# Optimization experiments

Measured on AMD Instinct MI355X. Metric: run time of the kernel, lower is better.

The kernel has to match this reference:

```python
import jax, jax.numpy as jnp
import numpy as np

B, T, U = 1024, 256, 256  # batch, timesteps, units (= input_dim)


def setup_inputs() -> dict:
    key = jax.random.key(0)
    ks = jax.random.split(key, 8)
    g = lambda k, shape: (jax.random.normal(k, shape, dtype=jnp.float32)
                          * np.float32(np.sqrt(2.0 / sum(shape if len(shape) > 1 else (shape[0], 1)))))
    return {
        "inputs": jax.random.normal(ks[0], (B, T, U), dtype=jnp.float32),
        "embedding_kernel": g(ks[1], (U, U)),
        "state_kernel": g(ks[2], (U, U)),
        "bias": g(ks[3], (U,)),
        "length_kernel": g(ks[4], (U, 1)),
        "rnn_state_kernel": g(ks[5], (U, 3 * U)),
        "rnn_embedding_kernel": g(ks[6], (U, 3 * U)),
        "rnn_newin_kernel": g(ks[7], (U, 3 * U)),
    }


def reference(inputs, embedding_kernel, state_kernel, bias, length_kernel,
              rnn_state_kernel, rnn_embedding_kernel, rnn_newin_kernel):
    u = state_kernel.shape[0]
    b = inputs.shape[0]

    def step(carry, x):
        state, s1, s2 = carry                       # each (B, U)
        query = state @ state_kernel                # (B, U)
        value = jnp.stack([s1, s2, x], axis=1)      # (B, 3, U) -- 3 memory slots
        emb = jnp.einsum('bsu,uv->bsv', value, embedding_kernel)
        act = jnp.tanh(emb + query[:, None, :] + bias)          # (B, 3, U)
        scores = jnp.einsum('bsu,u->bs', act, length_kernel[:, 0])  # (B, 3)
        prob = jax.nn.softmax(scores, axis=1)
        attention_out = jnp.einsum('bsu,bs->bu', value, prob)   # (B, U)

        gs = state @ rnn_state_kernel               # (B, 3U)
        ge = attention_out @ rnn_embedding_kernel   # (B, 3U)
        gn = x @ rnn_newin_kernel                   # (B, 3U)
        u_p = jax.nn.sigmoid(gs[:, :u] + ge[:, :u] + gn[:, :u])
        r_p = jax.nn.sigmoid(gs[:, u:2*u] + ge[:, u:2*u] + gn[:, u:2*u])
        cand = jnp.tanh(r_p * gs[:, 2*u:] + ge[:, 2*u:] + gn[:, 2*u:])
        step_out = (1.0 - u_p) * state + u_p * cand
        # state update mirrors Keras: [step_out, states[2], step_in]
        return (step_out, s2, x), None

    init = (jnp.zeros((b, u), inputs.dtype),
            jnp.zeros((b, u), inputs.dtype),
            jnp.zeros((b, u), inputs.dtype))
    xs = jnp.swapaxes(inputs, 0, 1)  # (T, B, U)
    (last_out, _, _), _ = jax.lax.scan(step, init, xs)
    return last_out  # (B, U) -- K.rnn's last_output
```

## Files before the change

kernel.cpp:

```cpp
#include <hip/hip_runtime.h>


typedef _Float16 f16;
typedef _Float16 f16x8 __attribute__((ext_vector_type(8)));
typedef _Float16 f16x4 __attribute__((ext_vector_type(4)));
typedef float f32x4 __attribute__((ext_vector_type(4)));

static __device__ __forceinline__ f32x4 mfma16(f16x8 a, f16x8 b, f32x4 c){
  return __builtin_amdgcn_mfma_f32_16x16x32_f16(a, b, c, 0, 0, 0);
}
static __device__ __forceinline__ float sigmoid_f(float x){
  return 1.0f / (1.0f + __expf(-x));
}
static __device__ __forceinline__ float tanh_f(float x){
  float e = __expf(2.0f * x);
  return 1.0f - 2.0f / (e + 1.0f);
}
static __device__ __forceinline__ void lgkm_barrier(){
  asm volatile("s_waitcnt lgkmcnt(0)" ::: "memory");
  __builtin_amdgcn_s_barrier();
}

__global__ void cast_w_kernel(const float* __restrict__ EK, const float* __restrict__ RE,
    const float* __restrict__ NW, const float* __restrict__ SK, const float* __restrict__ RS,
    f16* __restrict__ WcatT, f16* __restrict__ WsrF){
  int tid = blockIdx.x * 256 + threadIdx.x;
  if (tid < 458752){
    int n = tid >> 8, k = tid & 255;
    float v;
    if (n < 256)       v = EK[k*256 + n];
    else if (n < 1024) v = RE[k*768 + (n-256)];
    else               v = NW[k*768 + (n-1024)];
    WcatT[n*256 + k] = (f16)v;
  } else {
    int idx = tid - 458752;
    int e    = idx & 7;
    int lane = (idx >> 3) & 63;
    int kt   = (idx >> 9) & 7;
    int ct   = idx >> 12;
    int col  = ct*16 + (lane & 15);
    int k    = kt*32 + ((lane >> 4) & 3)*8 + e;
    float v = (col < 256) ? SK[k*256 + col] : RS[k*768 + (col-256)];
    WsrF[idx] = (f16)v;
  }
}

__global__ __launch_bounds__(256, 2) void gemm_f16_kernel(
    const float* __restrict__ X, const f16* __restrict__ Bm,
    f16* __restrict__ C, int Mtiles, int t_start)
{
  __shared__ f16 As[128*64];
  __shared__ f16 Bs[128*64];
  const int NT = 14;
  const int nwg = Mtiles * NT;
  int bid = blockIdx.x, wg = bid;
  if ((nwg & 7) == 0){ int cpx = nwg >> 3; wg = (bid & 7) * cpx + (bid >> 3); }
  const int mt = wg / NT, nt = wg % NT;
  const int tsl = mt >> 3;
  const int b0  = (mt & 7) * 128;
  const int t   = t_start + tsl;
  const int n0  = nt * 128;
  const int tid = threadIdx.x;
  const int l = tid & 63, wid = tid >> 6;
  const int wr = wid >> 1, wc = wid & 1;
  const int srow = tid >> 3;
  const int scol = (tid & 7) * 8;

  const size_t ASTR = 32ull * 65536ull;
  const float* Ab = X + ((size_t)(b0 + srow) * 256 + t) * 256 + scol;
  const f16*   Bb = Bm + ((size_t)(n0 + srow)) * 256 + scol;

  f16x8 ra[4], rb[4];
  #pragma unroll
  for (int j = 0; j < 4; ++j){
    f32x4 v0 = *(const f32x4*)(Ab + (size_t)j * ASTR);
    f32x4 v1 = *(const f32x4*)(Ab + (size_t)j * ASTR + 4);
    f16x8 h;
    #pragma unroll
    for (int jj = 0; jj < 8; ++jj) h[jj] = (f16)((jj < 4) ? v0[jj] : v1[jj-4]);
    ra[j] = h;
    rb[j] = *(const f16x8*)(Bb + (size_t)j * 32 * 256);
  }

  f32x4 acc[4][4];
  #pragma unroll
  for (int mi = 0; mi < 4; ++mi)
    #pragma unroll
    for (int ni = 0; ni < 4; ++ni)
      acc[mi][ni] = (f32x4){0.f,0.f,0.f,0.f};

  for (int kt = 0; kt < 4; ++kt){
    #pragma unroll
    for (int j = 0; j < 4; ++j){
      int row = srow + j*32;
      int e = (row*64 + scol) ^ ((row & 7) << 3);
      *(f16x8*)&As[e] = ra[j];
      *(f16x8*)&Bs[e] = rb[j];
    }
    __syncthreads();
    if (kt < 3){
      #pragma unroll
      for (int j = 0; j < 4; ++j){
        f32x4 v0 = *(const f32x4*)(Ab + (kt+1)*64 + (size_t)j * ASTR);
        f32x4 v1 = *(const f32x4*)(Ab + (kt+1)*64 + (size_t)j * ASTR + 4);
        f16x8 h;
        #pragma unroll
        for (int jj = 0; jj < 8; ++jj) h[jj] = (f16)((jj < 4) ? v0[jj] : v1[jj-4]);
        ra[j] = h;
        rb[j] = *(const f16x8*)(Bb + (kt+1)*64 + (size_t)j * 32 * 256);
      }
    }
    #pragma unroll
    for (int kk = 0; kk < 2; ++kk){
      f16x8 af[4], bfr[4];
      #pragma unroll
      for (int mi = 0; mi < 4; ++mi){
        int row = wr*64 + mi*16 + (l & 15);
        int e = (row*64 + kk*32 + (l >> 4)*8) ^ ((row & 7) << 3);
        af[mi] = *(const f16x8*)&As[e];
      }
      #pragma unroll
      for (int ni = 0; ni < 4; ++ni){
        int row = wc*64 + ni*16 + (l & 15);
        int e = (row*64 + kk*32 + (l >> 4)*8) ^ ((row & 7) << 3);
        bfr[ni] = *(const f16x8*)&Bs[e];
      }
      #pragma unroll
      for (int mi = 0; mi < 4; ++mi)
        #pragma unroll
        for (int ni = 0; ni < 4; ++ni)
          acc[mi][ni] = mfma16(af[mi], bfr[ni], acc[mi][ni]);
    }
    __syncthreads();
  }
  const size_t m0 = (size_t)mt * 128;
  #pragma unroll
  for (int mi = 0; mi < 4; ++mi){
    #pragma unroll
    for (int ni = 0; ni < 4; ++ni){
      int col = n0 + wc*64 + ni*16 + (l & 15);
      size_t row = m0 + wr*64 + mi*16 + ((l >> 4) * 4);
      #pragma unroll
      for (int j = 0; j < 4; ++j)
        C[(row + j) * 1792 + col] = (f16)acc[mi][ni][j];
    }
  }
}

__global__ __launch_bounds__(512, 1) void recurrent_kernel(
    const f16* __restrict__ P, const f16* __restrict__ WsrF,
    const float* __restrict__ bias, const float* __restrict__ Lk,
    float* __restrict__ state, float* __restrict__ out,
    int t0, int nsteps)
{
  __shared__ f16 Wl[8*8192];
  __shared__ f16 qg16[8*1032];
  __shared__ f16 stA[8*520];
  __shared__ __align__(16) float sb[256];
  __shared__ __align__(16) float sl[256];

  const int tid = threadIdx.x;
  const int l = tid & 63, w = tid >> 6;
  const int r0 = blockIdx.x * 8;
  const int arow = l & 15, agrp = l >> 4;
  const int c4 = l * 4;
  const int gb = r0 + w;
  const size_t SL = 1024ull*1792ull;
  const size_t gbo = (size_t)gb*1792;

  if (tid < 256){ sb[tid] = bias[tid]; sl[tid] = Lk[tid]; }
  for (int j = tid; j < 8*520; j += 512) stA[j] = (f16)0.f;

  const f16* const wbase = WsrF + (size_t)w*32768 + l*8;
  f16x8 Wreg[8][6];
  #pragma unroll
  for (int ct = 0; ct < 8; ++ct)
    #pragma unroll
    for (int kt = 0; kt < 6; ++kt)
      Wreg[ct][kt] = *(const f16x8*)(wbase + (ct*8 + kt)*512);
  #pragma unroll
  for (int ct = 0; ct < 8; ++ct)
    #pragma unroll
    for (int k2 = 0; k2 < 2; ++k2)
      *(f16x8*)&Wl[w*8192 + (ct*2 + k2)*512 + l*8] =
          *(const f16x8*)(wbase + (ct*8 + 6 + k2)*512);
  __syncthreads();

  f32x4 sn = *(const f32x4*)(state + (size_t)gb*256 + c4);
  f16* const sa = &stA[(l >> 3)*520 + ((((l >> 1) & 3) << 4) + w)*8 + (l & 1)*4];
  { f16x4 h; h[0]=(f16)sn[0]; h[1]=(f16)sn[1]; h[2]=(f16)sn[2]; h[3]=(f16)sn[3]; *(f16x4*)sa = h; }
  lgkm_barrier();

  for (int i = 0; i < nsteps; ++i){
    const int t = t0 + i;
    const f16* p2 = P + (size_t)(i+2)*SL + gbo;
    const f16* p1 = P + (size_t)(i+1)*SL + gbo;
    const f16* p0 = P + (size_t)(i+0)*SL + gbo;

    #pragma unroll
    for (int ct = 0; ct < 8; ++ct)
      #pragma unroll
      for (int kt = 0; kt < 6; ++kt)
        asm volatile("" : "+v"(Wreg[ct][kt]));

    const f16x4 cE2 = *(const f16x4*)(p2 + c4);

    f32x4 acc[8];
    #pragma unroll
    for (int c = 0; c < 8; ++c) acc[c] = (f32x4){0.f,0.f,0.f,0.f};
    {
      f16x8 av0 = *(const f16x8*)&stA[0*520 + l*8];
      f16x8 av1 = *(const f16x8*)&stA[1*520 + l*8];
      #pragma unroll
      for (int kt = 0; kt < 8; ++kt){
        const f16x8 avc = (kt & 1) ? av1 : av0;
        if (kt < 6){
          f16x8 nx = *(const f16x8*)&stA[(kt+2)*520 + l*8];
          if (kt & 1) av1 = nx; else av0 = nx;
        }
        #pragma unroll
        for (int ct = 0; ct < 8; ++ct){
          f16x8 B = (kt < 6) ? Wreg[ct][kt]
                             : *(const f16x8*)&Wl[w*8192 + (ct*2 + (kt-6))*512 + l*8];
          acc[ct] = mfma16(avc, B, acc[ct]);
        }
      }
    }

    const f16x4 cU  = *(const f16x4*)(p2 +  256 + c4);
    const f16x4 cR  = *(const f16x4*)(p2 +  512 + c4);
    const f16x4 cC  = *(const f16x4*)(p2 +  768 + c4);
    const f16x4 cNU = *(const f16x4*)(p2 + 1024 + c4);
    const f16x4 cNR = *(const f16x4*)(p2 + 1280 + c4);
    const f16x4 cNC = *(const f16x4*)(p2 + 1536 + c4);

    if (agrp < 2){
      #pragma unroll
      for (int ct = 0; ct < 8; ++ct){
        #pragma unroll
        for (int j = 0; j < 4; ++j)
          qg16[(agrp*4 + j)*1032 + w*128 + ct*16 + arow] = (f16)acc[ct][j];
      }
    }
    lgkm_barrier();

    const f16x4 E0 = *(const f16x4*)(p0 + c4);
    const f16x4 E1 = *(const f16x4*)(p1 + c4);
    const f16x4 U1 = *(const f16x4*)(p1 + 256 + c4);
    const f16x4 R1 = *(const f16x4*)(p1 + 512 + c4);
    const f16x4 C1 = *(const f16x4*)(p1 + 768 + c4);
    const f16x4 U2 = *(const f16x4*)(p0 + 256 + c4);
    const f16x4 R2 = *(const f16x4*)(p0 + 512 + c4);
    const f16x4 C2 = *(const f16x4*)(p0 + 768 + c4);

    const f16x4 qv = *(const f16x4*)&qg16[w*1032 + c4];
    const f16x4 qu = *(const f16x4*)&qg16[w*1032 + 256 + c4];
    const f16x4 qr = *(const f16x4*)&qg16[w*1032 + 512 + c4];
    const f16x4 qc = *(const f16x4*)&qg16[w*1032 + 768 + c4];
    const f32x4 bb = *(const f32x4*)&sb[c4];
    const f32x4 lk = *(const f32x4*)&sl[c4];
    float s0 = 0.f, s1 = 0.f, s2 = 0.f;
    #pragma unroll
    for (int j = 0; j < 4; ++j){
      const float qb = (float)qv[j] + bb[j];
      s0 += tanh_f((float)E0[j]  + qb) * lk[j];
      s1 += tanh_f((float)E1[j]  + qb) * lk[j];
      s2 += tanh_f((float)cE2[j] + qb) * lk[j];
    }
    #pragma unroll
    for (int off = 32; off; off >>= 1){
      s0 += __shfl_xor(s0, off);
      s1 += __shfl_xor(s1, off);
      s2 += __shfl_xor(s2, off);
    }
    const float mx = fmaxf(fmaxf(s0, s1), s2);
    const float x0 = __expf(s0 - mx), x1 = __expf(s1 - mx), x2 = __expf(s2 - mx);
    const float inv = 1.0f / (x0 + x1 + x2);
    const float pr0 = x0*inv, pr1 = x1*inv, pr2 = x2*inv;

    #pragma unroll
    for (int j = 0; j < 4; ++j){
      const float geu = pr2*(float)cU[j] + pr1*(float)U1[j] + pr0*(float)U2[j];
      const float ger = pr2*(float)cR[j] + pr1*(float)R1[j] + pr0*(float)R2[j];
      const float gec = pr2*(float)cC[j] + pr1*(float)C1[j] + pr0*(float)C2[j];
      const float up   = sigmoid_f((float)qu[j] + geu + (float)cNU[j]);
      const float rp   = sigmoid_f((float)qr[j] + ger + (float)cNR[j]);
      const float cand = tanh_f(rp*(float)qc[j] + gec + (float)cNC[j]);
      sn[j] = (1.0f - up)*sn[j] + up*cand;
    }
    { f16x4 h; h[0]=(f16)sn[0]; h[1]=(f16)sn[1]; h[2]=(f16)sn[2]; h[3]=(f16)sn[3]; *(f16x4*)sa = h; }
    if (t == 255) *(f32x4*)(out + (size_t)gb*256 + c4) = sn;
    lgkm_barrier();
  }

  *(f32x4*)(state + (size_t)gb*256 + c4) = sn;
}

extern "C" void kernel_launch(void* const* d_in, const int* in_sizes, int n_in,
                              void* d_out, int out_size, void* d_ws, size_t ws_size,
                              hipStream_t stream)
{
  const float* X  = (const float*)d_in[0];
  const float* EK = (const float*)d_in[1];
  const float* SK = (const float*)d_in[2];
  const float* BI = (const float*)d_in[3];
  const float* LK = (const float*)d_in[4];
  const float* RS = (const float*)d_in[5];
  const float* RE = (const float*)d_in[6];
  const float* NW = (const float*)d_in[7];
  float* out = (float*)d_out;
  char* ws = (char*)d_ws;

  const size_t slabB = 1024ull * 1792ull * 2ull;
  const size_t wB    = 917504ull + 524288ull + 1048576ull;
  int CT = 4;
  if      (ws_size >= 34ull*slabB + wB) CT = 32;
  else if (ws_size >= 18ull*slabB + wB) CT = 16;
  else if (ws_size >= 10ull*slabB + wB) CT = 8;

  f16* P = (f16*)ws;
  size_t poff = (size_t)(CT + 2) * slabB;
  f16* WcatT = (f16*)(ws + poff);
  f16* WsrF  = (f16*)(ws + poff + 917504ull);
  float* state = (float*)(ws + poff + 917504ull + 524288ull);

  hipMemsetAsync(state, 0, 1048576ull, stream);
  hipMemsetAsync(P, 0, 2ull*slabB, stream);
  cast_w_kernel<<<2816, 256, 0, stream>>>(EK, RE, NW, SK, RS, WcatT, WsrF);

  const int nch = 256 / CT;
  for (int c = 0; c < nch; ++c){
    const int t0 = c * CT;
    const int t_start  = (c == 0) ? 0 : (t0 - 2);
    const int slab_off = (c == 0) ? 2 : 0;
    const int Mtiles = (((c == 0) ? CT : (CT + 2)) * 1024) / 128;
    gemm_f16_kernel<<<Mtiles * 14, 256, 0, stream>>>(
        X, WcatT, P + (size_t)slab_off * 1024 * 1792, Mtiles, t_start);
    recurrent_kernel<<<128, 512, 0, stream>>>(P, WsrF, BI, LK, state, out, t0, CT);
  }
}
```

Baseline: 1.875 ms.

## Halve rows per recurrent block, split each row across two waves, double grid

The recurrent kernel now handles 4 batch rows per block instead of 8, with two waves sharing each row's 256 units. It launches 256 blocks, so more CUs are busy during the serial time loop. The attention score reduction gains a cross-wave step through shared memory and an extra barrier per timestep. Global loads are moved earlier to overlap with the MFMA phase. A larger chunk size of 64 timesteps is also allowed when the workspace is big enough, which cuts launch count.

```diff
diff --git a/kernel.cpp b/kernel.cpp
--- a/kernel.cpp
+++ b/kernel.cpp
@@ -4,7 +4,9 @@
 typedef _Float16 f16;
 typedef _Float16 f16x8 __attribute__((ext_vector_type(8)));
 typedef _Float16 f16x4 __attribute__((ext_vector_type(4)));
+typedef _Float16 f16x2 __attribute__((ext_vector_type(2)));
 typedef float f32x4 __attribute__((ext_vector_type(4)));
+typedef float f32x2 __attribute__((ext_vector_type(2)));
 
 static __device__ __forceinline__ f32x4 mfma16(f16x8 a, f16x8 b, f32x4 c){
   return __builtin_amdgcn_mfma_f32_16x16x32_f16(a, b, c, 0, 0, 0);
@@ -154,17 +156,19 @@
     int t0, int nsteps)
 {
   __shared__ f16 Wl[8*8192];
-  __shared__ f16 qg16[8*1032];
+  __shared__ f16 qg16[4*1032];
   __shared__ f16 stA[8*520];
   __shared__ __align__(16) float sb[256];
   __shared__ __align__(16) float sl[256];
+  __shared__ float sp[4][2][3];
 
   const int tid = threadIdx.x;
   const int l = tid & 63, w = tid >> 6;
-  const int r0 = blockIdx.x * 8;
+  const int r0 = blockIdx.x * 4;
   const int arow = l & 15, agrp = l >> 4;
-  const int c4 = l * 4;
-  const int gb = r0 + w;
+  const int r = w >> 1, h = w & 1;
+  const int c2 = h*128 + l*2;
+  const int gb = r0 + r;
   const size_t SL = 1024ull*1792ull;
   const size_t gbo = (size_t)gb*1792;
 
@@ -186,9 +190,10 @@
           *(const f16x8*)(wbase + (ct*8 + 6 + k2)*512);
   __syncthreads();
 
-  f32x4 sn = *(const f32x4*)(state + (size_t)gb*256 + c4);
-  f16* const sa = &stA[(l >> 3)*520 + ((((l >> 1) & 3) << 4) + w)*8 + (l & 1)*4];
-  { f16x4 h; h[0]=(f16)sn[0]; h[1]=(f16)sn[1]; h[2]=(f16)sn[2]; h[3]=(f16)sn[3]; *(f16x4*)sa = h; }
+  f32x2 sn = *(const f32x2*)(state + (size_t)gb*256 + c2);
+  const int kt0 = c2 >> 5, g0 = (c2 >> 3) & 3, e0 = c2 & 7;
+  f16* const sa = &stA[kt0*520 + (g0*16 + r)*8 + e0];
+  { f16x2 hh; hh[0]=(f16)sn[0]; hh[1]=(f16)sn[1]; *(f16x2*)sa = hh; }
   lgkm_barrier();
 
   for (int i = 0; i < nsteps; ++i){
@@ -203,7 +208,15 @@
       for (int kt = 0; kt < 6; ++kt)
         asm volatile("" : "+v"(Wreg[ct][kt]));
 
-    const f16x4 cE2 = *(const f16x4*)(p2 + c4);
+    const f16x2 cE2 = *(const f16x2*)(p2 + c2);
+    const f16x2 cU  = *(const f16x2*)(p2 +  256 + c2);
+    const f16x2 cR  = *(const f16x2*)(p2 +  512 + c2);
+    const f16x2 cC  = *(const f16x2*)(p2 +  768 + c2);
+    const f16x2 cNU = *(const f16x2*)(p2 + 1024 + c2);
+    const f16x2 cNR = *(const f16x2*)(p2 + 1280 + c2);
+    const f16x2 cNC = *(const f16x2*)(p2 + 1536 + c2);
+    const f16x2 E0  = *(const f16x2*)(p0 + c2);
+    const f16x2 E1  = *(const f16x2*)(p1 + c2);
 
     f32x4 acc[8];
     #pragma unroll
@@ -227,73 +240,74 @@
       }
     }
 
-    const f16x4 cU  = *(const f16x4*)(p2 +  256 + c4);
-    const f16x4 cR  = *(const f16x4*)(p2 +  512 + c4);
-    const f16x4 cC  = *(const f16x4*)(p2 +  768 + c4);
-    const f16x4 cNU = *(const f16x4*)(p2 + 1024 + c4);
-    const f16x4 cNR = *(const f16x4*)(p2 + 1280 + c4);
-    const f16x4 cNC = *(const f16x4*)(p2 + 1536 + c4);
-
-    if (agrp < 2){
+    if (agrp == 0){
       #pragma unroll
       for (int ct = 0; ct < 8; ++ct){
         #pragma unroll
         for (int j = 0; j < 4; ++j)
-          qg16[(agrp*4 + j)*1032 + w*128 + ct*16 + arow] = (f16)acc[ct][j];
+          qg16[j*1032 + w*128 + ct*16 + arow] = (f16)acc[ct][j];
       }
     }
     lgkm_barrier();
 
-    const f16x4 E0 = *(const f16x4*)(p0 + c4);
-    const f16x4 E1 = *(const f16x4*)(p1 + c4);
-    const f16x4 U1 = *(const f16x4*)(p1 + 256 + c4);
-    const f16x4 R1 = *(const f16x4*)(p1 + 512 + c4);
-    const f16x4 C1 = *(const f16x4*)(p1 + 768 + c4);
-    const f16x4 U2 = *(const f16x4*)(p0 + 256 + c4);
-    const f16x4 R2 = *(const f16x4*)(p0 + 512 + c4);
-    const f16x4 C2 = *(const f16x4*)(p0 + 768 + c4);
-
-    const f16x4 qv = *(const f16x4*)&qg16[w*1032 + c4];
-    const f16x4 qu = *(const f16x4*)&qg16[w*1032 + 256 + c4];
-    const f16x4 qr = *(const f16x4*)&qg16[w*1032 + 512 + c4];
-    const f16x4 qc = *(const f16x4*)&qg16[w*1032 + 768 + c4];
-    const f32x4 bb = *(const f32x4*)&sb[c4];
-    const f32x4 lk = *(const f32x4*)&sl[c4];
-    float s0 = 0.f, s1 = 0.f, s2 = 0.f;
-    #pragma unroll
-    for (int j = 0; j < 4; ++j){
-      const float qb = (float)qv[j] + bb[j];
-      s0 += tanh_f((float)E0[j]  + qb) * lk[j];
-      s1 += tanh_f((float)E1[j]  + qb) * lk[j];
-      s2 += tanh_f((float)cE2[j] + qb) * lk[j];
-    }
-    #pragma unroll
-    for (int off = 32; off; off >>= 1){
-      s0 += __shfl_xor(s0, off);
-      s1 += __shfl_xor(s1, off);
-      s2 += __shfl_xor(s2, off);
-    }
-    const float mx = fmaxf(fmaxf(s0, s1), s2);
-    const float x0 = __expf(s0 - mx), x1 = __expf(s1 - mx), x2 = __expf(s2 - mx);
-    const float inv = 1.0f / (x0 + x1 + x2);
-    const float pr0 = x0*inv, pr1 = x1*inv, pr2 = x2*inv;
-
-    #pragma unroll
-    for (int j = 0; j < 4; ++j){
-      const float geu = pr2*(float)cU[j] + pr1*(float)U1[j] + pr0*(float)U2[j];
-      const float ger = pr2*(float)cR[j] + pr1*(float)R1[j] + pr0*(float)R2[j];
-      const float gec = pr2*(float)cC[j] + pr1*(float)C1[j] + pr0*(float)C2[j];
-      const float up   = sigmoid_f((float)qu[j] + geu + (float)cNU[j]);
-      const float rp   = sigmoid_f((float)qr[j] + ger + (float)cNR[j]);
-      const float cand = tanh_f(rp*(float)qc[j] + gec + (float)cNC[j]);
-      sn[j] = (1.0f - up)*sn[j] + up*cand;
-    }
-    { f16x4 h; h[0]=(f16)sn[0]; h[1]=(f16)sn[1]; h[2]=(f16)sn[2]; h[3]=(f16)sn[3]; *(f16x4*)sa = h; }
-    if (t == 255) *(f32x4*)(out + (size_t)gb*256 + c4) = sn;
+    const f16x2 U1 = *(const f16x2*)(p1 + 256 + c2);
+    const f16x2 R1 = *(const f16x2*)(p1 + 512 + c2);
+    const f16x2 C1 = *(const f16x2*)(p1 + 768 + c2);
+    const f16x2 U2 = *(const f16x2*)(p0 + 256 + c2);
+    const f16x2 R2 = *(const f16x2*)(p0 + 512 + c2);
+    const f16x2 C2 = *(const f16x2*)(p0 + 768 + c2);
+
+    {
+      const f16x2 qv = *(const f16x2*)&qg16[r*1032 + c2];
+      const f32x2 bb = *(const f32x2*)&sb[c2];
+      const f32x2 lk = *(const f32x2*)&sl[c2];
+      float s0 = 0.f, s1 = 0.f, s2 = 0.f;
+      #pragma unroll
+      for (int j = 0; j < 2; ++j){
+        const float qb = (float)qv[j] + bb[j];
+        s0 += tanh_f((float)E0[j]  + qb) * lk[j];
+        s1 += tanh_f((float)E1[j]  + qb) * lk[j];
+        s2 += tanh_f((float)cE2[j] + qb) * lk[j];
+      }
+      #pragma unroll
+      for (int off = 32; off; off >>= 1){
+        s0 += __shfl_xor(s0, off);
+        s1 += __shfl_xor(s1, off);
+        s2 += __shfl_xor(s2, off);
+      }
+      if (l == 0){ sp[r][h][0] = s0; sp[r][h][1] = s1; sp[r][h][2] = s2; }
+    }
     lgkm_barrier();
-  }
-
-  *(f32x4*)(state + (size_t)gb*256 + c4) = sn;
+
+    {
+      const float s0 = sp[r][0][0] + sp[r][1][0];
+      const float s1 = sp[r][0][1] + sp[r][1][1];
+      const float s2 = sp[r][0][2] + sp[r][1][2];
+      const float mx = fmaxf(fmaxf(s0, s1), s2);
+      const float x0 = __expf(s0 - mx), x1 = __expf(s1 - mx), x2 = __expf(s2 - mx);
+      const float inv = 1.0f / (x0 + x1 + x2);
+      const float pr0 = x0*inv, pr1 = x1*inv, pr2 = x2*inv;
+
+      const f16x2 qu = *(const f16x2*)&qg16[r*1032 + 256 + c2];
+      const f16x2 qr = *(const f16x2*)&qg16[r*1032 + 512 + c2];
+      const f16x2 qc = *(const f16x2*)&qg16[r*1032 + 768 + c2];
+      #pragma unroll
+      for (int j = 0; j < 2; ++j){
+        const float geu = pr2*(float)cU[j] + pr1*(float)U1[j] + pr0*(float)U2[j];
+        const float ger = pr2*(float)cR[j] + pr1*(float)R1[j] + pr0*(float)R2[j];
+        const float gec = pr2*(float)cC[j] + pr1*(float)C1[j] + pr0*(float)C2[j];
+        const float up   = sigmoid_f((float)qu[j] + geu + (float)cNU[j]);
+        const float rp   = sigmoid_f((float)qr[j] + ger + (float)cNR[j]);
+        const float cand = tanh_f(rp*(float)qc[j] + gec + (float)cNC[j]);
+        sn[j] = (1.0f - up)*sn[j] + up*cand;
+      }
+      { f16x2 hh; hh[0]=(f16)sn[0]; hh[1]=(f16)sn[1]; *(f16x2*)sa = hh; }
+      if (t == 255) *(f32x2*)(out + (size_t)gb*256 + c2) = sn;
+    }
+    lgkm_barrier();
+  }
+
+  *(f32x2*)(state + (size_t)gb*256 + c2) = sn;
 }
 
 extern "C" void kernel_launch(void* const* d_in, const int* in_sizes, int n_in,
@@ -314,7 +328,8 @@
   const size_t slabB = 1024ull * 1792ull * 2ull;
   const size_t wB    = 917504ull + 524288ull + 1048576ull;
   int CT = 4;
-  if      (ws_size >= 34ull*slabB + wB) CT = 32;
+  if      (ws_size >= 66ull*slabB + wB) CT = 64;
+  else if (ws_size >= 34ull*slabB + wB) CT = 32;
   else if (ws_size >= 18ull*slabB + wB) CT = 16;
   else if (ws_size >= 10ull*slabB + wB) CT = 8;
 
@@ -336,6 +351,6 @@
     const int Mtiles = (((c == 0) ? CT : (CT + 2)) * 1024) / 128;
     gemm_f16_kernel<<<Mtiles * 14, 256, 0, stream>>>(
         X, WcatT, P + (size_t)slab_off * 1024 * 1792, Mtiles, t_start);
-    recurrent_kernel<<<128, 512, 0, stream>>>(P, WsrF, BI, LK, state, out, t0, CT);
-  }
-}
+    recurrent_kernel<<<256, 512, 0, stream>>>(P, WsrF, BI, LK, state, out, t0, CT);
+  }
+}
```

Result: faster. 1.724 ms (-8.1%).
